# Kernel optimization log

Hardware: AMD Instinct MI355X
Metric: run time of the kernel (lower is better)

Reference implementation:

```python
import jax, jax.numpy as jnp
import numpy as np

N_NODES = 50000
N_EDGES = 1600000
IN_DIM = 128
OUT_DIM = 64
HEADS = 4


def setup_inputs() -> dict:
    key = jax.random.key(0)
    k1, k2, k3, k4 = jax.random.split(key, 4)
    x = jax.random.normal(k1, (N_NODES, IN_DIM), dtype=jnp.float32)
    edge_index = jax.random.randint(k2, (2, N_EDGES), 0, N_NODES, dtype=jnp.int64)
    # W[h]: per-head linear weight (in_dim -> out_dim), no bias
    W = jax.random.normal(k3, (HEADS, IN_DIM, OUT_DIM), dtype=jnp.float32) * 0.1
    # a[h]: attention vector over concat([h_src, h_dst]) -> scalar, no bias
    a = jax.random.normal(k4, (HEADS, 2 * OUT_DIM), dtype=jnp.float32) * 0.1
    return {"x": x, "edge_index": edge_index, "W": W, "a": a}


def reference(x, edge_index, W, a):
    n_nodes = x.shape[0]
    out_dim = W.shape[2]
    src, dst = edge_index[0], edge_index[1]
    # per-head projection: [N, H, O]
    h = jnp.einsum('nf,hfo->nho', x, W)
    h_src = h[src]  # [E, H, O]
    h_dst = h[dst]  # [E, H, O]
    a_src, a_dst = a[:, :out_dim], a[:, out_dim:]  # split of concat weight
    # e = leaky_relu(a^T [h_src || h_dst]) per edge, per head: [E, H]
    e = jnp.einsum('eho,ho->eh', h_src, a_src) + jnp.einsum('eho,ho->eh', h_dst, a_dst)
    e = jax.nn.leaky_relu(e, negative_slope=0.01)
    # NOTE: faithful to source — softmax over ALL edges (dim=0), not per-dst
    alpha = jax.nn.softmax(e, axis=0)  # [E, H]
    msgs = h_src * alpha[:, :, None]  # [E, H, O]
    agg = jax.ops.segment_sum(msgs, dst, num_segments=n_nodes)  # [N, H, O]
    # concat heads along feature dim (head-major), matching torch.cat(out, dim=1)
    return agg.reshape(n_nodes, -1)
```

## Files before the change

kernel.cpp:

```cpp
#include <hip/hip_runtime.h>
#include <stdint.h>

#define N_NODES 50000
#define N_EDGES 1600000
#define IN_DIM  128
#define OUT_DIM 64
#define HEADS   4
#define HO      (HEADS*OUT_DIM)

typedef __attribute__((ext_vector_type(8))) short short8;
typedef __attribute__((ext_vector_type(8))) unsigned short bf16x8;
typedef __attribute__((ext_vector_type(4))) float f32x4;

__device__ __forceinline__ unsigned fenc(float f) {
    unsigned u = __float_as_uint(f);
    return (u & 0x80000000u) ? ~u : (u | 0x80000000u);
}
__device__ __forceinline__ float fdec(unsigned u) {
    return __uint_as_float((u & 0x80000000u) ? (u ^ 0x80000000u) : ~u);
}
__device__ __forceinline__ float lrelu(float v) {
    return v >= 0.f ? v : 0.01f * v;
}
__device__ __forceinline__ unsigned short f2bf(float f) {
    unsigned u = __float_as_uint(f);
    return (unsigned short)((u + 0x7FFFu + ((u >> 16) & 1u)) >> 16);
}
__device__ __forceinline__ float bf2f(unsigned short b) {
    return __uint_as_float(((unsigned)b) << 16);
}

#define HIST_BLOCKS  1024
#define XCONV_BLOCKS 1024
#define WT_BLOCKS    32

__global__ __launch_bounds__(256) void k_prep_hist(
    const float* __restrict__ x, const float* __restrict__ W,
    const int* __restrict__ edst,
    unsigned short* __restrict__ xb, unsigned short* __restrict__ wt,
    int* __restrict__ cnt, int* __restrict__ rank)
{
    int b = blockIdx.x;
    if (b < HIST_BLOCKS) {
        const int stride = HIST_BLOCKS * 256;
        for (int e = b * 256 + threadIdx.x; e < N_EDGES; e += stride)
            rank[e] = atomicAdd(&cnt[edst[e]], 1);
        return;
    }
    b -= HIST_BLOCKS;
    if (b < XCONV_BLOCKS) {
        const int total4 = N_NODES * IN_DIM / 4;
        const int stride = XCONV_BLOCKS * 256;
        for (int i = b * 256 + threadIdx.x; i < total4; i += stride) {
            float4 v = ((const float4*)x)[i];
            ushort4 u;
            u.x = f2bf(v.x); u.y = f2bf(v.y); u.z = f2bf(v.z); u.w = f2bf(v.w);
            ((ushort4*)xb)[i] = u;
        }
        return;
    }
    b -= XCONV_BLOCKS;
    {
        int item = b * 256 + threadIdx.x;
        int n  = item >> 5;
        int k0 = (item & 31) * 4;
        int h = n >> 6, o = n & 63;
        const float* wp = &W[((size_t)h * IN_DIM + k0) * OUT_DIM + o];
        ushort4 u;
        u.x = f2bf(wp[0 * OUT_DIM]);
        u.y = f2bf(wp[1 * OUT_DIM]);
        u.z = f2bf(wp[2 * OUT_DIM]);
        u.w = f2bf(wp[3 * OUT_DIM]);
        *(ushort4*)&wt[(size_t)n * IN_DIM + k0] = u;
    }
}

#define BM 64
#define GEMM_BLOCKS ((N_NODES + BM - 1) / BM)

__global__ __launch_bounds__(256) void k_gemm(
    const unsigned short* __restrict__ xb, const unsigned short* __restrict__ wt,
    const float* __restrict__ a,
    unsigned short* __restrict__ hb, float* __restrict__ s_src, float* __restrict__ s_dst)
{
    extern __shared__ char smem[];
    char* Alds = smem;
    char* Blds = smem + 16384;

    const int tid  = threadIdx.x;
    const int wave = tid >> 6;
    const int lane = tid & 63;
    const int node0 = blockIdx.x * BM;

    {
        const char* xsrc = (const char*)xb + (size_t)node0 * 256;
        #pragma unroll
        for (int j = 0; j < 4; ++j) {
            int o = (j * 256 + tid) * 16;
            uint4 v = *(const uint4*)(xsrc + o);
            int sw = o ^ (((o >> 8) & 7) << 4);
            *(uint4*)(Alds + sw) = v;
        }
    }
    {
        const char* wsrc = (const char*)wt;
        #pragma unroll
        for (int j = 0; j < 16; ++j) {
            int o = (j * 256 + tid) * 16;
            uint4 v = *(const uint4*)(wsrc + o);
            int sw = o ^ (((o >> 8) & 7) << 4);
            *(uint4*)(Blds + sw) = v;
        }
    }
    __syncthreads();

    const int wr0  = wave * 16;
    const int l15  = lane & 15;
    const int lhi  = lane >> 4;
    const int kxor = (lane & 7) << 4;

    short8 af[4];
    #pragma unroll
    for (int s = 0; s < 4; ++s)
        af[s] = *(const short8*)(Alds + (wr0 + l15) * 256 + ((s * 64 + lhi * 16) ^ kxor));

    f32x4 acc[16];
    #pragma unroll
    for (int nt = 0; nt < 16; ++nt) acc[nt] = (f32x4){0.f, 0.f, 0.f, 0.f};

    #pragma unroll
    for (int nt = 0; nt < 16; ++nt) {
        const char* bbase = Blds + (nt * 16 + l15) * 256;
        #pragma unroll
        for (int s = 0; s < 4; ++s) {
            short8 bf = *(const short8*)(bbase + ((s * 64 + lhi * 16) ^ kxor));
            acc[nt] = __builtin_amdgcn_mfma_f32_16x16x32_bf16(af[s], bf, acc[nt], 0, 0, 0);
        }
    }

    #pragma unroll
    for (int nt = 0; nt < 16; ++nt) {
        int col = nt * 16 + l15;
        #pragma unroll
        for (int r = 0; r < 4; ++r) {
            int node = node0 + wr0 + lhi * 4 + r;
            if (node < N_NODES)
                hb[(size_t)node * HO + col] = f2bf(acc[nt][r]);
        }
    }

    #pragma unroll
    for (int h = 0; h < 4; ++h) {
        float avs0 = a[h*128 +  0 + l15], avs1 = a[h*128 + 16 + l15];
        float avs2 = a[h*128 + 32 + l15], avs3 = a[h*128 + 48 + l15];
        float avd0 = a[h*128 + 64 + l15], avd1 = a[h*128 + 80 + l15];
        float avd2 = a[h*128 + 96 + l15], avd3 = a[h*128 + 112 + l15];
        #pragma unroll
        for (int r = 0; r < 4; ++r) {
            float vs = acc[4*h+0][r]*avs0 + acc[4*h+1][r]*avs1
                     + acc[4*h+2][r]*avs2 + acc[4*h+3][r]*avs3;
            float vd = acc[4*h+0][r]*avd0 + acc[4*h+1][r]*avd1
                     + acc[4*h+2][r]*avd2 + acc[4*h+3][r]*avd3;
            #pragma unroll
            for (int m = 8; m >= 1; m >>= 1) {
                vs += __shfl_xor(vs, m);
                vd += __shfl_xor(vd, m);
            }
            int node = node0 + wr0 + lhi * 4 + r;
            if (l15 == 0 && node < N_NODES) {
                s_src[node * HEADS + h] = vs;
                s_dst[node * HEADS + h] = vd;
            }
        }
    }
}

__global__ __launch_bounds__(1024) void k_scan(
    const int* __restrict__ cnt, int* __restrict__ row_start)
{
    __shared__ int part[1024];
    const int t  = threadIdx.x;
    const int CH = (N_NODES + 1023) / 1024;
    const int lo = t * CH;
    const int hi = (lo + CH < N_NODES) ? lo + CH : N_NODES;

    int s = 0;
    for (int i = lo; i < hi; ++i) s += cnt[i];
    part[t] = s;
    __syncthreads();

    for (int off = 1; off < 1024; off <<= 1) {
        int v = (t >= off) ? part[t - off] : 0;
        __syncthreads();
        part[t] += v;
        __syncthreads();
    }

    int run = (t == 0) ? 0 : part[t - 1];
    for (int i = lo; i < hi; ++i) {
        row_start[i] = run;
        run += cnt[i];
    }
    if (t == 1023) row_start[N_NODES] = part[1023];
}

__global__ __launch_bounds__(256) void k_nodemax(
    const float* __restrict__ s_src, const float* __restrict__ s_dst,
    unsigned* __restrict__ gmax_src, unsigned* __restrict__ gmax_dst)
{
    float4 ms = make_float4(-1e30f, -1e30f, -1e30f, -1e30f);
    float4 md = ms;
    const int stride = gridDim.x * blockDim.x;
    for (int n = blockIdx.x * blockDim.x + threadIdx.x; n < N_NODES; n += stride) {
        float4 vs = ((const float4*)s_src)[n];
        float4 vd = ((const float4*)s_dst)[n];
        ms.x = fmaxf(ms.x, vs.x); ms.y = fmaxf(ms.y, vs.y);
        ms.z = fmaxf(ms.z, vs.z); ms.w = fmaxf(ms.w, vs.w);
        md.x = fmaxf(md.x, vd.x); md.y = fmaxf(md.y, vd.y);
        md.z = fmaxf(md.z, vd.z); md.w = fmaxf(md.w, vd.w);
    }
    #pragma unroll
    for (int m = 32; m >= 1; m >>= 1) {
        ms.x = fmaxf(ms.x, __shfl_xor(ms.x, m)); ms.y = fmaxf(ms.y, __shfl_xor(ms.y, m));
        ms.z = fmaxf(ms.z, __shfl_xor(ms.z, m)); ms.w = fmaxf(ms.w, __shfl_xor(ms.w, m));
        md.x = fmaxf(md.x, __shfl_xor(md.x, m)); md.y = fmaxf(md.y, __shfl_xor(md.y, m));
        md.z = fmaxf(md.z, __shfl_xor(md.z, m)); md.w = fmaxf(md.w, __shfl_xor(md.w, m));
    }
    if ((threadIdx.x & 63) == 0) {
        atomicMax(&gmax_src[0], fenc(ms.x)); atomicMax(&gmax_src[1], fenc(ms.y));
        atomicMax(&gmax_src[2], fenc(ms.z)); atomicMax(&gmax_src[3], fenc(ms.w));
        atomicMax(&gmax_dst[0], fenc(md.x)); atomicMax(&gmax_dst[1], fenc(md.y));
        atomicMax(&gmax_dst[2], fenc(md.z)); atomicMax(&gmax_dst[3], fenc(md.w));
    }
}

#define BUCKET_BLOCKS 512
__global__ __launch_bounds__(256) void k_bucket(
    const int* __restrict__ esrc, const int* __restrict__ edst,
    const int* __restrict__ rank, const int* __restrict__ row_start,
    const float* __restrict__ s_src, const float* __restrict__ s_dst,
    const unsigned* __restrict__ gmax_src, const unsigned* __restrict__ gmax_dst,
    unsigned* __restrict__ rec, double* __restrict__ gsum)
{
    const float mx0 = lrelu(fdec(gmax_src[0]) + fdec(gmax_dst[0]));
    const float mx1 = lrelu(fdec(gmax_src[1]) + fdec(gmax_dst[1]));
    const float mx2 = lrelu(fdec(gmax_src[2]) + fdec(gmax_dst[2]));
    const float mx3 = lrelu(fdec(gmax_src[3]) + fdec(gmax_dst[3]));
    double a0 = 0.0, a1 = 0.0, a2 = 0.0, a3 = 0.0;
    const int stride = gridDim.x * blockDim.x;
    for (int e = blockIdx.x * blockDim.x + threadIdx.x; e < N_EDGES; e += stride) {
        int s = esrc[e], d = edst[e];
        int pos = row_start[d] + rank[e];
        float4 ss = *(const float4*)&s_src[s * HEADS];
        float4 sd = *(const float4*)&s_dst[d * HEADS];
        unsigned b0 = f2bf(__expf(lrelu(ss.x + sd.x) - mx0));
        unsigned b1 = f2bf(__expf(lrelu(ss.y + sd.y) - mx1));
        unsigned b2 = f2bf(__expf(lrelu(ss.z + sd.z) - mx2));
        unsigned b3 = f2bf(__expf(lrelu(ss.w + sd.w) - mx3));
        rec[(size_t)pos * 3 + 0] = (unsigned)s;
        rec[(size_t)pos * 3 + 1] = b0 | (b1 << 16);
        rec[(size_t)pos * 3 + 2] = b2 | (b3 << 16);
        a0 += (double)bf2f((unsigned short)b0);
        a1 += (double)bf2f((unsigned short)b1);
        a2 += (double)bf2f((unsigned short)b2);
        a3 += (double)bf2f((unsigned short)b3);
    }
    #pragma unroll
    for (int m = 32; m >= 1; m >>= 1) {
        a0 += __shfl_xor(a0, m); a1 += __shfl_xor(a1, m);
        a2 += __shfl_xor(a2, m); a3 += __shfl_xor(a3, m);
    }
    __shared__ double part[4][4];
    const int wave = threadIdx.x >> 6;
    if ((threadIdx.x & 63) == 0) {
        part[wave][0] = a0; part[wave][1] = a1; part[wave][2] = a2; part[wave][3] = a3;
    }
    __syncthreads();
    if (threadIdx.x < 4) {
        double t = part[0][threadIdx.x] + part[1][threadIdx.x]
                 + part[2][threadIdx.x] + part[3][threadIdx.x];
        atomicAdd(&gsum[threadIdx.x], t);
    }
}

__global__ __launch_bounds__(256) void k_agg(
    const int* __restrict__ row_start, const unsigned* __restrict__ rec,
    const unsigned short* __restrict__ hb,
    const double* __restrict__ gsum, float* __restrict__ out)
{
    const int wid = (int)((blockIdx.x * 256u + threadIdx.x) >> 6);
    if (wid >= N_NODES) return;
    const int lane = threadIdx.x & 63;
    const int half = lane >> 5;
    const int l32  = lane & 31;
    const int head = l32 >> 3;
    const int og   = (l32 & 7) * 8;
    const int hoff = head * OUT_DIM + og;

    const int beg = row_start[wid];
    const int end = row_start[wid + 1];
    const float inv = (float)(1.0 / gsum[head]);

    float c0=0.f,c1=0.f,c2=0.f,c3=0.f,c4=0.f,c5=0.f,c6=0.f,c7=0.f;

    #define EDGE(rc)                                                            \
        {                                                                       \
            unsigned aw = (head & 2) ? (rc).z : (rc).y;                         \
            float p = bf2f((unsigned short)((head & 1) ? (aw >> 16)             \
                                                       : (aw & 0xFFFFu)));      \
            bf16x8 u = *(const bf16x8*)&hb[(size_t)(rc).x * HO + hoff];         \
            c0 = fmaf(p, bf2f(u[0]), c0); c1 = fmaf(p, bf2f(u[1]), c1);         \
            c2 = fmaf(p, bf2f(u[2]), c2); c3 = fmaf(p, bf2f(u[3]), c3);         \
            c4 = fmaf(p, bf2f(u[4]), c4); c5 = fmaf(p, bf2f(u[5]), c5);         \
            c6 = fmaf(p, bf2f(u[6]), c6); c7 = fmaf(p, bf2f(u[7]), c7);         \
        }

    int j = beg + half;
    for (; j + 6 < end; j += 8) {
        uint3 rA = *(const uint3*)&rec[(size_t)j * 3];
        uint3 rB = *(const uint3*)&rec[(size_t)(j + 2) * 3];
        uint3 rC = *(const uint3*)&rec[(size_t)(j + 4) * 3];
        uint3 rD = *(const uint3*)&rec[(size_t)(j + 6) * 3];
        EDGE(rA); EDGE(rB); EDGE(rC); EDGE(rD);
    }
    for (; j < end; j += 2) {
        uint3 rA = *(const uint3*)&rec[(size_t)j * 3];
        EDGE(rA);
    }
    #undef EDGE

    c0 += __shfl_xor(c0, 32); c1 += __shfl_xor(c1, 32);
    c2 += __shfl_xor(c2, 32); c3 += __shfl_xor(c3, 32);
    c4 += __shfl_xor(c4, 32); c5 += __shfl_xor(c5, 32);
    c6 += __shfl_xor(c6, 32); c7 += __shfl_xor(c7, 32);

    float4 v = half ? make_float4(c4 * inv, c5 * inv, c6 * inv, c7 * inv)
                    : make_float4(c0 * inv, c1 * inv, c2 * inv, c3 * inv);
    *(float4*)&out[(size_t)wid * HO + hoff + half * 4] = v;
}

extern "C" void kernel_launch(void* const* d_in, const int* in_sizes, int n_in,
                              void* d_out, int out_size, void* d_ws, size_t ws_size,
                              hipStream_t stream)
{
    const float* x    = (const float*)d_in[0];
    const int*   eidx = (const int*)d_in[1];
    const float* W    = (const float*)d_in[2];
    const float* a    = (const float*)d_in[3];
    float* out = (float*)d_out;

    unsigned short* hb = (unsigned short*)d_ws;
    unsigned short* xb = hb + (size_t)N_NODES * HO;
    unsigned short* wt = xb + (size_t)N_NODES * IN_DIM;
    float*    s_src    = (float*)(wt + (size_t)HO * IN_DIM);
    float*    s_dst    = s_src + (size_t)N_NODES * HEADS;
    double*   gsum     = (double*)(s_dst + (size_t)N_NODES * HEADS);
    unsigned* gmax_src = (unsigned*)(gsum + 4);
    unsigned* gmax_dst = gmax_src + 4;
    int*      cnt      = (int*)(gmax_dst + 4);
    int*      row_start = cnt + N_NODES;
    int*      rank     = row_start + (N_NODES + 2);
    unsigned* rec      = (unsigned*)(rank + N_EDGES);

    const int* esrc = eidx;
    const int* edst = eidx + N_EDGES;

    hipMemsetAsync(gsum, 0, 4 * sizeof(double) + 8 * sizeof(unsigned) + N_NODES * sizeof(int),
                   stream);

    k_prep_hist<<<HIST_BLOCKS + XCONV_BLOCKS + WT_BLOCKS, 256, 0, stream>>>(
        x, W, edst, xb, wt, cnt, rank);
    k_gemm<<<GEMM_BLOCKS, 256, 81920, stream>>>(xb, wt, a, hb, s_src, s_dst);
    k_scan<<<1, 1024, 0, stream>>>(cnt, row_start);
    k_nodemax<<<64, 256, 0, stream>>>(s_src, s_dst, gmax_src, gmax_dst);
    k_bucket<<<BUCKET_BLOCKS, 256, 0, stream>>>(
        esrc, edst, rank, row_start, s_src, s_dst, gmax_src, gmax_dst, rec, gsum);
    k_agg<<<(N_NODES * 64 + 255) / 256, 256, 0, stream>>>(
        row_start, rec, hb, gsum, out);
}
```

Measured before the change: 354.1 us.

## Fuse x-to-bf16 conversion into GEMM, merge scan with node-max, spread gsum atomics

```diff
diff --git a/kernel.cpp b/kernel.cpp
--- a/kernel.cpp
+++ b/kernel.cpp
@@ -12,13 +12,6 @@
 typedef __attribute__((ext_vector_type(8))) unsigned short bf16x8;
 typedef __attribute__((ext_vector_type(4))) float f32x4;
 
-__device__ __forceinline__ unsigned fenc(float f) {
-    unsigned u = __float_as_uint(f);
-    return (u & 0x80000000u) ? ~u : (u | 0x80000000u);
-}
-__device__ __forceinline__ float fdec(unsigned u) {
-    return __uint_as_float((u & 0x80000000u) ? (u ^ 0x80000000u) : ~u);
-}
 __device__ __forceinline__ float lrelu(float v) {
     return v >= 0.f ? v : 0.01f * v;
 }
@@ -30,76 +23,64 @@
     return __uint_as_float(((unsigned)b) << 16);
 }
 
-#define HIST_BLOCKS  1024
-#define XCONV_BLOCKS 1024
-#define WT_BLOCKS    32
-
-__global__ __launch_bounds__(256) void k_prep_hist(
-    const float* __restrict__ x, const float* __restrict__ W,
-    const int* __restrict__ edst,
-    unsigned short* __restrict__ xb, unsigned short* __restrict__ wt,
-    int* __restrict__ cnt, int* __restrict__ rank)
-{
-    int b = blockIdx.x;
-    if (b < HIST_BLOCKS) {
+__global__ __launch_bounds__(256) void k_prep_wt(
+    const float* __restrict__ W, unsigned short* __restrict__ wt)
+{
+    int item = blockIdx.x * 256 + threadIdx.x;
+    int n  = item >> 5;
+    int k0 = (item & 31) * 4;
+    int h = n >> 6, o = n & 63;
+    const float* wp = &W[((size_t)h * IN_DIM + k0) * OUT_DIM + o];
+    ushort4 u;
+    u.x = f2bf(wp[0 * OUT_DIM]);
+    u.y = f2bf(wp[1 * OUT_DIM]);
+    u.z = f2bf(wp[2 * OUT_DIM]);
+    u.w = f2bf(wp[3 * OUT_DIM]);
+    *(ushort4*)&wt[(size_t)n * IN_DIM + k0] = u;
+}
+
+#define HIST_BLOCKS 1024
+#define BM 64
+#define GEMM_BLOCKS ((N_NODES + BM - 1) / BM)
+
+__global__ __launch_bounds__(256) void k_gemm_hist(
+    const float* __restrict__ x, const unsigned short* __restrict__ wt,
+    const float* __restrict__ a, const int* __restrict__ edst,
+    int* __restrict__ cnt, int* __restrict__ rank,
+    unsigned short* __restrict__ hb, float* __restrict__ s_src, float* __restrict__ s_dst)
+{
+    extern __shared__ char smem[];
+
+    if (blockIdx.x < HIST_BLOCKS) {
         const int stride = HIST_BLOCKS * 256;
-        for (int e = b * 256 + threadIdx.x; e < N_EDGES; e += stride)
+        for (int e = blockIdx.x * 256 + threadIdx.x; e < N_EDGES; e += stride)
             rank[e] = atomicAdd(&cnt[edst[e]], 1);
         return;
     }
-    b -= HIST_BLOCKS;
-    if (b < XCONV_BLOCKS) {
-        const int total4 = N_NODES * IN_DIM / 4;
-        const int stride = XCONV_BLOCKS * 256;
-        for (int i = b * 256 + threadIdx.x; i < total4; i += stride) {
-            float4 v = ((const float4*)x)[i];
-            ushort4 u;
-            u.x = f2bf(v.x); u.y = f2bf(v.y); u.z = f2bf(v.z); u.w = f2bf(v.w);
-            ((ushort4*)xb)[i] = u;
-        }
-        return;
-    }
-    b -= XCONV_BLOCKS;
-    {
-        int item = b * 256 + threadIdx.x;
-        int n  = item >> 5;
-        int k0 = (item & 31) * 4;
-        int h = n >> 6, o = n & 63;
-        const float* wp = &W[((size_t)h * IN_DIM + k0) * OUT_DIM + o];
-        ushort4 u;
-        u.x = f2bf(wp[0 * OUT_DIM]);
-        u.y = f2bf(wp[1 * OUT_DIM]);
-        u.z = f2bf(wp[2 * OUT_DIM]);
-        u.w = f2bf(wp[3 * OUT_DIM]);
-        *(ushort4*)&wt[(size_t)n * IN_DIM + k0] = u;
-    }
-}
-
-#define BM 64
-#define GEMM_BLOCKS ((N_NODES + BM - 1) / BM)
-
-__global__ __launch_bounds__(256) void k_gemm(
-    const unsigned short* __restrict__ xb, const unsigned short* __restrict__ wt,
-    const float* __restrict__ a,
-    unsigned short* __restrict__ hb, float* __restrict__ s_src, float* __restrict__ s_dst)
-{
-    extern __shared__ char smem[];
+
     char* Alds = smem;
     char* Blds = smem + 16384;
 
     const int tid  = threadIdx.x;
     const int wave = tid >> 6;
     const int lane = tid & 63;
-    const int node0 = blockIdx.x * BM;
+    const int node0 = (blockIdx.x - HIST_BLOCKS) * BM;
 
     {
-        const char* xsrc = (const char*)xb + (size_t)node0 * 256;
         #pragma unroll
         for (int j = 0; j < 4; ++j) {
-            int o = (j * 256 + tid) * 16;
-            uint4 v = *(const uint4*)(xsrc + o);
+            int o    = (j * 256 + tid) * 16;
+            int row  = o >> 8;
+            int fcol = (o & 255) >> 1;
+            int node = node0 + row;
+            const float* sp = x + (size_t)(node < N_NODES ? node : N_NODES - 1) * IN_DIM + fcol;
+            float4 v0 = *(const float4*)sp;
+            float4 v1 = *(const float4*)(sp + 4);
+            bf16x8 u;
+            u[0] = f2bf(v0.x); u[1] = f2bf(v0.y); u[2] = f2bf(v0.z); u[3] = f2bf(v0.w);
+            u[4] = f2bf(v1.x); u[5] = f2bf(v1.y); u[6] = f2bf(v1.z); u[7] = f2bf(v1.w);
             int sw = o ^ (((o >> 8) & 7) << 4);
-            *(uint4*)(Alds + sw) = v;
+            *(bf16x8*)(Alds + sw) = u;
         }
     }
     {
@@ -175,43 +156,43 @@
     }
 }
 
-__global__ __launch_bounds__(1024) void k_scan(
-    const int* __restrict__ cnt, int* __restrict__ row_start)
-{
-    __shared__ int part[1024];
-    const int t  = threadIdx.x;
-    const int CH = (N_NODES + 1023) / 1024;
-    const int lo = t * CH;
-    const int hi = (lo + CH < N_NODES) ? lo + CH : N_NODES;
-
-    int s = 0;
-    for (int i = lo; i < hi; ++i) s += cnt[i];
-    part[t] = s;
-    __syncthreads();
-
-    for (int off = 1; off < 1024; off <<= 1) {
-        int v = (t >= off) ? part[t - off] : 0;
+__global__ __launch_bounds__(1024) void k_mid(
+    const int* __restrict__ cnt, int* __restrict__ row_start,
+    const float* __restrict__ s_src, const float* __restrict__ s_dst,
+    float* __restrict__ gmax)
+{
+    if (blockIdx.x == 0) {
+        __shared__ int part[1024];
+        const int t  = threadIdx.x;
+        const int CH = (N_NODES + 1023) / 1024;
+        const int lo = t * CH;
+        const int hi = (lo + CH < N_NODES) ? lo + CH : N_NODES;
+
+        int s = 0;
+        for (int i = lo; i < hi; ++i) s += cnt[i];
+        part[t] = s;
         __syncthreads();
-        part[t] += v;
-        __syncthreads();
-    }
-
-    int run = (t == 0) ? 0 : part[t - 1];
-    for (int i = lo; i < hi; ++i) {
-        row_start[i] = run;
-        run += cnt[i];
-    }
-    if (t == 1023) row_start[N_NODES] = part[1023];
-}
-
-__global__ __launch_bounds__(256) void k_nodemax(
-    const float* __restrict__ s_src, const float* __restrict__ s_dst,
-    unsigned* __restrict__ gmax_src, unsigned* __restrict__ gmax_dst)
-{
+
+        for (int off = 1; off < 1024; off <<= 1) {
+            int v = (t >= off) ? part[t - off] : 0;
+            __syncthreads();
+            part[t] += v;
+            __syncthreads();
+        }
+
+        int run = (t == 0) ? 0 : part[t - 1];
+        for (int i = lo; i < hi; ++i) {
+            row_start[i] = run;
+            run += cnt[i];
+        }
+        if (t == 1023) row_start[N_NODES] = part[1023];
+        return;
+    }
+
+    __shared__ float red[16][8];
     float4 ms = make_float4(-1e30f, -1e30f, -1e30f, -1e30f);
     float4 md = ms;
-    const int stride = gridDim.x * blockDim.x;
-    for (int n = blockIdx.x * blockDim.x + threadIdx.x; n < N_NODES; n += stride) {
+    for (int n = threadIdx.x; n < N_NODES; n += 1024) {
         float4 vs = ((const float4*)s_src)[n];
         float4 vd = ((const float4*)s_dst)[n];
         ms.x = fmaxf(ms.x, vs.x); ms.y = fmaxf(ms.y, vs.y);
@@ -226,26 +207,32 @@
         md.x = fmaxf(md.x, __shfl_xor(md.x, m)); md.y = fmaxf(md.y, __shfl_xor(md.y, m));
         md.z = fmaxf(md.z, __shfl_xor(md.z, m)); md.w = fmaxf(md.w, __shfl_xor(md.w, m));
     }
+    const int w = threadIdx.x >> 6;
     if ((threadIdx.x & 63) == 0) {
-        atomicMax(&gmax_src[0], fenc(ms.x)); atomicMax(&gmax_src[1], fenc(ms.y));
-        atomicMax(&gmax_src[2], fenc(ms.z)); atomicMax(&gmax_src[3], fenc(ms.w));
-        atomicMax(&gmax_dst[0], fenc(md.x)); atomicMax(&gmax_dst[1], fenc(md.y));
-        atomicMax(&gmax_dst[2], fenc(md.z)); atomicMax(&gmax_dst[3], fenc(md.w));
-    }
-}
-
-#define BUCKET_BLOCKS 512
+        red[w][0] = ms.x; red[w][1] = ms.y; red[w][2] = ms.z; red[w][3] = ms.w;
+        red[w][4] = md.x; red[w][5] = md.y; red[w][6] = md.z; red[w][7] = md.w;
+    }
+    __syncthreads();
+    if (threadIdx.x < 8) {
+        float m = red[0][threadIdx.x];
+        #pragma unroll
+        for (int k = 1; k < 16; ++k) m = fmaxf(m, red[k][threadIdx.x]);
+        gmax[threadIdx.x] = m;
+    }
+}
+
+#define BUCKET_BLOCKS 256
 __global__ __launch_bounds__(256) void k_bucket(
     const int* __restrict__ esrc, const int* __restrict__ edst,
     const int* __restrict__ rank, const int* __restrict__ row_start,
     const float* __restrict__ s_src, const float* __restrict__ s_dst,
-    const unsigned* __restrict__ gmax_src, const unsigned* __restrict__ gmax_dst,
+    const float* __restrict__ gmax,
     unsigned* __restrict__ rec, double* __restrict__ gsum)
 {
-    const float mx0 = lrelu(fdec(gmax_src[0]) + fdec(gmax_dst[0]));
-    const float mx1 = lrelu(fdec(gmax_src[1]) + fdec(gmax_dst[1]));
-    const float mx2 = lrelu(fdec(gmax_src[2]) + fdec(gmax_dst[2]));
-    const float mx3 = lrelu(fdec(gmax_src[3]) + fdec(gmax_dst[3]));
+    const float mx0 = lrelu(gmax[0] + gmax[4]);
+    const float mx1 = lrelu(gmax[1] + gmax[5]);
+    const float mx2 = lrelu(gmax[2] + gmax[6]);
+    const float mx3 = lrelu(gmax[3] + gmax[7]);
     double a0 = 0.0, a1 = 0.0, a2 = 0.0, a3 = 0.0;
     const int stride = gridDim.x * blockDim.x;
     for (int e = blockIdx.x * blockDim.x + threadIdx.x; e < N_EDGES; e += stride) {
@@ -279,7 +266,7 @@
     if (threadIdx.x < 4) {
         double t = part[0][threadIdx.x] + part[1][threadIdx.x]
                  + part[2][threadIdx.x] + part[3][threadIdx.x];
-        atomicAdd(&gsum[threadIdx.x], t);
+        atomicAdd(&gsum[(blockIdx.x & 7) * 4 + threadIdx.x], t);
     }
 }
 
@@ -299,35 +286,58 @@
 
     const int beg = row_start[wid];
     const int end = row_start[wid + 1];
-    const float inv = (float)(1.0 / gsum[head]);
+    double gs = 0.0;
+    #pragma unroll
+    for (int r = 0; r < 8; ++r) gs += gsum[r * 4 + head];
+    const float inv = (float)(1.0 / gs);
 
     float c0=0.f,c1=0.f,c2=0.f,c3=0.f,c4=0.f,c5=0.f,c6=0.f,c7=0.f;
 
-    #define EDGE(rc)                                                            \
-        {                                                                       \
-            unsigned aw = (head & 2) ? (rc).z : (rc).y;                         \
-            float p = bf2f((unsigned short)((head & 1) ? (aw >> 16)             \
-                                                       : (aw & 0xFFFFu)));      \
-            bf16x8 u = *(const bf16x8*)&hb[(size_t)(rc).x * HO + hoff];         \
-            c0 = fmaf(p, bf2f(u[0]), c0); c1 = fmaf(p, bf2f(u[1]), c1);         \
-            c2 = fmaf(p, bf2f(u[2]), c2); c3 = fmaf(p, bf2f(u[3]), c3);         \
-            c4 = fmaf(p, bf2f(u[4]), c4); c5 = fmaf(p, bf2f(u[5]), c5);         \
-            c6 = fmaf(p, bf2f(u[6]), c6); c7 = fmaf(p, bf2f(u[7]), c7);         \
-        }
+    #define ALPHA(rc) bf2f((unsigned short)((head & 1)                          \
+                        ? (((head & 2) ? (rc).z : (rc).y) >> 16)                \
+                        : (((head & 2) ? (rc).z : (rc).y) & 0xFFFFu)))
+    #define HROW(rc) (*(const bf16x8*)&hb[(size_t)(rc).x * HO + hoff])
+    #define ACC(p,u)                                                            \
+        { c0 = fmaf(p, bf2f((u)[0]), c0); c1 = fmaf(p, bf2f((u)[1]), c1);       \
+          c2 = fmaf(p, bf2f((u)[2]), c2); c3 = fmaf(p, bf2f((u)[3]), c3);       \
+          c4 = fmaf(p, bf2f((u)[4]), c4); c5 = fmaf(p, bf2f((u)[5]), c5);       \
+          c6 = fmaf(p, bf2f((u)[6]), c6); c7 = fmaf(p, bf2f((u)[7]), c7); }
 
     int j = beg + half;
+    for (; j + 14 < end; j += 16) {
+        uint3 rA = *(const uint3*)&rec[(size_t)j * 3];
+        uint3 rB = *(const uint3*)&rec[(size_t)(j + 2) * 3];
+        uint3 rC = *(const uint3*)&rec[(size_t)(j + 4) * 3];
+        uint3 rD = *(const uint3*)&rec[(size_t)(j + 6) * 3];
+        uint3 rE = *(const uint3*)&rec[(size_t)(j + 8) * 3];
+        uint3 rF = *(const uint3*)&rec[(size_t)(j + 10) * 3];
+        uint3 rG = *(const uint3*)&rec[(size_t)(j + 12) * 3];
+        uint3 rH = *(const uint3*)&rec[(size_t)(j + 14) * 3];
+        bf16x8 uA = HROW(rA), uB = HROW(rB), uC = HROW(rC), uD = HROW(rD);
+        bf16x8 uE = HROW(rE), uF = HROW(rF), uG = HROW(rG), uH = HROW(rH);
+        float pA = ALPHA(rA), pB = ALPHA(rB), pC = ALPHA(rC), pD = ALPHA(rD);
+        float pE = ALPHA(rE), pF = ALPHA(rF), pG = ALPHA(rG), pH = ALPHA(rH);
+        ACC(pA,uA); ACC(pB,uB); ACC(pC,uC); ACC(pD,uD);
+        ACC(pE,uE); ACC(pF,uF); ACC(pG,uG); ACC(pH,uH);
+    }
     for (; j + 6 < end; j += 8) {
         uint3 rA = *(const uint3*)&rec[(size_t)j * 3];
         uint3 rB = *(const uint3*)&rec[(size_t)(j + 2) * 3];
         uint3 rC = *(const uint3*)&rec[(size_t)(j + 4) * 3];
         uint3 rD = *(const uint3*)&rec[(size_t)(j + 6) * 3];
-        EDGE(rA); EDGE(rB); EDGE(rC); EDGE(rD);
+        bf16x8 uA = HROW(rA), uB = HROW(rB), uC = HROW(rC), uD = HROW(rD);
+        float pA = ALPHA(rA), pB = ALPHA(rB), pC = ALPHA(rC), pD = ALPHA(rD);
+        ACC(pA,uA); ACC(pB,uB); ACC(pC,uC); ACC(pD,uD);
     }
     for (; j < end; j += 2) {
         uint3 rA = *(const uint3*)&rec[(size_t)j * 3];
-        EDGE(rA);
-    }
-    #undef EDGE
+        bf16x8 uA = HROW(rA);
+        float pA = ALPHA(rA);
+        ACC(pA,uA);
+    }
+    #undef ALPHA
+    #undef HROW
+    #undef ACC
 
     c0 += __shfl_xor(c0, 32); c1 += __shfl_xor(c1, 32);
     c2 += __shfl_xor(c2, 32); c3 += __shfl_xor(c3, 32);
@@ -350,14 +360,12 @@
     float* out = (float*)d_out;
 
     unsigned short* hb = (unsigned short*)d_ws;
-    unsigned short* xb = hb + (size_t)N_NODES * HO;
-    unsigned short* wt = xb + (size_t)N_NODES * IN_DIM;
+    unsigned short* wt = hb + (size_t)N_NODES * HO;
     float*    s_src    = (float*)(wt + (size_t)HO * IN_DIM);
     float*    s_dst    = s_src + (size_t)N_NODES * HEADS;
     double*   gsum     = (double*)(s_dst + (size_t)N_NODES * HEADS);
-    unsigned* gmax_src = (unsigned*)(gsum + 4);
-    unsigned* gmax_dst = gmax_src + 4;
-    int*      cnt      = (int*)(gmax_dst + 4);
+    float*    gmax     = (float*)(gsum + 32);
+    int*      cnt      = (int*)(gmax + 8);
     int*      row_start = cnt + N_NODES;
     int*      rank     = row_start + (N_NODES + 2);
     unsigned* rec      = (unsigned*)(rank + N_EDGES);
@@ -365,16 +373,15 @@
     const int* esrc = eidx;
     const int* edst = eidx + N_EDGES;
 
-    hipMemsetAsync(gsum, 0, 4 * sizeof(double) + 8 * sizeof(unsigned) + N_NODES * sizeof(int),
+    hipMemsetAsync(gsum, 0, 32 * sizeof(double) + 8 * sizeof(float) + N_NODES * sizeof(int),
                    stream);
 
-    k_prep_hist<<<HIST_BLOCKS + XCONV_BLOCKS + WT_BLOCKS, 256, 0, stream>>>(
-        x, W, edst, xb, wt, cnt, rank);
-    k_gemm<<<GEMM_BLOCKS, 256, 81920, stream>>>(xb, wt, a, hb, s_src, s_dst);
-    k_scan<<<1, 1024, 0, stream>>>(cnt, row_start);
-    k_nodemax<<<64, 256, 0, stream>>>(s_src, s_dst, gmax_src, gmax_dst);
+    k_prep_wt<<<32, 256, 0, stream>>>(W, wt);
+    k_gemm_hist<<<HIST_BLOCKS + GEMM_BLOCKS, 256, 81920, stream>>>(
+        x, wt, a, edst, cnt, rank, hb, s_src, s_dst);
+    k_mid<<<2, 1024, 0, stream>>>(cnt, row_start, s_src, s_dst, gmax);
     k_bucket<<<BUCKET_BLOCKS, 256, 0, stream>>>(
-        esrc, edst, rank, row_start, s_src, s_dst, gmax_src, gmax_dst, rec, gsum);
+        esrc, edst, rank, row_start, s_src, s_dst, gmax, rec, gsum);
     k_agg<<<(N_NODES * 64 + 255) / 256, 256, 0, stream>>>(
         row_start, rec, hb, gsum, out);
 }
```

Result: faster. 318.7 us (-10.0%).
